# Optimization experiments

Measured on AMD Instinct MI355X. Metric: run time of the kernel, lower is better.

## Reference

```python
import jax, jax.numpy as jnp
import numpy as np

IMG_W, IMG_H = 960.0, 512.0          # NETWORK.IMAGE_SIZE
HM_W, HM_H = 240.0, 128.0            # NETWORK.HEATMAP_SIZE (w, h)
GRID_SIZE = (8000.0, 8000.0, 2000.0)
CUBE = (80, 80, 20)
SPACE_CENTER = (0.0, -500.0, 800.0)


def _make_grid():
    # compute_grid: meshgrid(indexing='ij'), flattened to [nbins, 3]
    gx = np.linspace(-GRID_SIZE[0] / 2, GRID_SIZE[0] / 2, CUBE[0]) + SPACE_CENTER[0]
    gy = np.linspace(-GRID_SIZE[1] / 2, GRID_SIZE[1] / 2, CUBE[1]) + SPACE_CENTER[1]
    gz = np.linspace(-GRID_SIZE[2] / 2, GRID_SIZE[2] / 2, CUBE[2]) + SPACE_CENTER[2]
    X, Y, Z = np.meshgrid(gx, gy, gz, indexing='ij')
    return jnp.asarray(np.stack([X.ravel(), Y.ravel(), Z.ravel()], 1), jnp.float32)


def setup_inputs() -> dict:
    key = jax.random.key(0)
    ks = jax.random.split(key, 8)
    n, B, J, H, W = 5, 4, 15, 128, 240
    heatmaps = jax.random.uniform(ks[0], (n, B, J, H, W), jnp.float32)
    # cameras: rotate about z per view, positioned so all grid points have depth > 0
    thetas = np.linspace(0.0, 2 * np.pi, n, endpoint=False)
    Rs = np.zeros((n, B, 3, 3), np.float32)
    for v, th in enumerate(thetas):
        c, s = np.cos(th), np.sin(th)
        Rs[v, :] = np.array([[c, -s, 0.0], [s, c, 0.0], [0.0, 0.0, 1.0]], np.float32)
    cam_R = jnp.asarray(Rs)
    cam_T = jnp.asarray(np.tile(np.array([0.0, 0.0, -5000.0], np.float32), (n, B, 1))) \
        + 50.0 * jax.random.normal(ks[1], (n, B, 3), jnp.float32)
    cam_f = 1500.0 + 20.0 * jax.random.normal(ks[2], (n, B, 2), jnp.float32)
    cam_c = jnp.asarray([IMG_W / 2, IMG_H / 2], jnp.float32) \
        + 5.0 * jax.random.normal(ks[3], (n, B, 2), jnp.float32)
    cam_k = jnp.asarray(np.tile(np.array([-0.01, 0.001, 0.0], np.float32), (n, B, 1))) \
        + 1e-4 * jax.random.normal(ks[4], (n, B, 3), jnp.float32)
    cam_p = 1e-3 * jax.random.normal(ks[5], (n, B, 2), jnp.float32)
    center = jnp.asarray([IMG_W / 2, IMG_H / 2], jnp.float32) \
        + 10.0 * jax.random.normal(ks[6], (n, B, 2), jnp.float32)
    scale = jnp.asarray([IMG_W / 200.0, IMG_H / 200.0], jnp.float32) \
        * (1.0 + 0.05 * jax.random.uniform(ks[7], (n, B, 2), jnp.float32))
    return {"heatmaps": heatmaps, "cam_R": cam_R, "cam_T": cam_T, "cam_f": cam_f,
            "cam_c": cam_c, "cam_k": cam_k, "cam_p": cam_p, "center": center,
            "scale": scale}


def _forward(heatmaps, cam_R, cam_T, cam_f, cam_c, cam_k, cam_p, center, scale):
    n, B, J, Hd, Wd = heatmaps.shape
    grid = _make_grid()                                   # [N, 3]
    N = grid.shape[0]
    # --- project_pose (pinhole + radial/tangential distortion) ---
    diff = grid[None, None] - cam_T[:, :, None, :]        # [v,b,N,3]
    xcam = jnp.einsum('vbij,vbnj->vbni', cam_R, diff)     # [v,b,N,3]
    y = xcam[..., :2] / (xcam[..., 2:3] + 1e-5)
    r2 = jnp.sum(y * y, -1)                               # [v,b,N]
    radial = 1.0 + cam_k[..., 0:1] * r2 + cam_k[..., 1:2] * r2 ** 2 + cam_k[..., 2:3] * r2 ** 3
    tan = cam_p[..., 0:1] * y[..., 1] + cam_p[..., 1:2] * y[..., 0]
    y = y * (radial + 2.0 * tan)[..., None] \
        + jnp.stack([cam_p[..., 1], cam_p[..., 0]], -1)[:, :, None, :] * r2[..., None]
    pix = cam_f[:, :, None, :] * y + cam_c[:, :, None, :]  # [v,b,N,2]
    # --- bounding: inside image of size (width, height) = 2*center ---
    wh = 2.0 * center                                      # [v,b,2]
    bounding = ((pix[..., 0] >= 0) & (pix[..., 1] >= 0)
                & (pix[..., 0] < wh[..., 0:1]) & (pix[..., 1] < wh[..., 1:2])
                ).astype(heatmaps.dtype)                   # [v,b,N]
    maxwh = jnp.maximum(wh[..., 0], wh[..., 1])[..., None, None]
    pix = jnp.clip(pix, -1.0, maxwh)
    # --- get_transform(center, scale, 0, img_size) + do_transform ---
    hs = 200.0 * scale                                     # [v,b,2]
    img = jnp.asarray([IMG_W, IMG_H], heatmaps.dtype)
    t_scale = img / hs                                     # diag of affine
    t_off = img * (-center / hs + 0.5)
    xy = pix * t_scale[:, :, None, :] + t_off[:, :, None, :]
    # scale to heatmap resolution, then to normalized [-1,1] (align_corners=True)
    xy = xy * (jnp.asarray([HM_W, HM_H], heatmaps.dtype) / img)
    sg = xy / jnp.asarray([HM_W - 1, HM_H - 1], heatmaps.dtype) * 2.0 - 1.0
    sg = jnp.clip(sg, -1.1, 1.1)
    # --- bilinear grid_sample, align_corners=True, zeros padding ---
    px = (sg[..., 0] + 1.0) * 0.5 * (Wd - 1)
    py = (sg[..., 1] + 1.0) * 0.5 * (Hd - 1)
    x0 = jnp.floor(px)
    y0 = jnp.floor(py)
    wx = px - x0
    wy = py - y0
    x0i = x0.astype(jnp.int32)
    y0i = y0.astype(jnp.int32)
    flat = heatmaps.reshape(n, B, J, Hd * Wd)

    def corner(xi, yi):
        valid = ((xi >= 0) & (xi < Wd) & (yi >= 0) & (yi < Hd)).astype(heatmaps.dtype)
        idx = jnp.clip(yi, 0, Hd - 1) * Wd + jnp.clip(xi, 0, Wd - 1)   # [v,b,N]
        g = jnp.take_along_axis(flat, idx[:, :, None, :], axis=3)       # [v,b,J,N]
        return g * valid[:, :, None, :]

    val = (corner(x0i, y0i) * ((1 - wx) * (1 - wy))[:, :, None, :]
           + corner(x0i + 1, y0i) * (wx * (1 - wy))[:, :, None, :]
           + corner(x0i, y0i + 1) * ((1 - wx) * wy)[:, :, None, :]
           + corner(x0i + 1, y0i + 1) * (wx * wy)[:, :, None, :])       # [v,b,J,N]
    # --- per-view cube = bounding * sampled; combine over views ---
    cubes_v = bounding[:, :, None, :] * val
    num = jnp.sum(cubes_v * bounding[:, :, None, :], axis=0)            # [b,J,N]
    den = jnp.sum(bounding, axis=0)[:, None, :] + 1e-6
    cubes = jnp.clip(num / den, 0.0, 1.0).reshape(B, J, CUBE[0], CUBE[1], CUBE[2])
    grids = jnp.broadcast_to(grid, (B, N, 3))
    return cubes, grids


def reference(heatmaps, cam_R, cam_T, cam_f, cam_c, cam_k, cam_p, center, scale):
    return _forward(heatmaps, cam_R, cam_T, cam_f, cam_c, cam_k, cam_p, center, scale)
```

## Files before the change

### kernel.cpp

```cpp
#include <hip/hip_runtime.h>
#include <hip/hip_fp16.h>

#define NV 5
#define NB 4
#define NJ 15
#define HD 128
#define WD 240
#define CX 80
#define CY 80
#define CZ 20
#define NPTS (CX*CY*CZ)
#define JP16 16
#define BLOCKS_PER_B (NPTS/256)
#define NWG (NB*BLOCKS_PER_B)

struct ViewSample {
    float w[4];
    int   cx0, cx1, cy0, cy1;
    float bnd;
};

__device__ __forceinline__ ViewSample project_one_view(
    float gx, float gy, float gz,
    const float* __restrict__ cam_R, const float* __restrict__ cam_T,
    const float* __restrict__ cam_f, const float* __restrict__ cam_c,
    const float* __restrict__ cam_k, const float* __restrict__ cam_p,
    const float* __restrict__ center, const float* __restrict__ scale,
    int cb)
{
    const float* R = cam_R + cb*9;
    const float* T = cam_T + cb*3;
    float fx = cam_f[cb*2+0], fy = cam_f[cb*2+1];
    float ccx = cam_c[cb*2+0], ccy = cam_c[cb*2+1];
    float k0 = cam_k[cb*3+0], k1 = cam_k[cb*3+1], k2 = cam_k[cb*3+2];
    float p0 = cam_p[cb*2+0], p1 = cam_p[cb*2+1];
    float cenx = center[cb*2+0], ceny = center[cb*2+1];
    float scx = scale[cb*2+0],  scy = scale[cb*2+1];

    float dx = gx - T[0], dy = gy - T[1], dz = gz - T[2];
    float xc = R[0]*dx + R[1]*dy + R[2]*dz;
    float yc = R[3]*dx + R[4]*dy + R[5]*dz;
    float zc = R[6]*dx + R[7]*dy + R[8]*dz;
    float invz = 1.0f / (zc + 1e-5f);
    float ux = xc * invz, uy = yc * invz;
    float r2 = ux*ux + uy*uy;
    float radial = 1.0f + k0*r2 + k1*(r2*r2) + k2*(r2*r2*r2);
    float tn = p0*uy + p1*ux;
    float m  = radial + 2.0f*tn;
    float xd = ux*m + p1*r2;
    float yd = uy*m + p0*r2;
    float pixx = fx*xd + ccx;
    float pixy = fy*yd + ccy;

    float whx = 2.0f*cenx, why = 2.0f*ceny;
    float bnd = (pixx >= 0.0f && pixy >= 0.0f && pixx < whx && pixy < why) ? 1.0f : 0.0f;
    float mwh = fmaxf(whx, why);
    pixx = fminf(fmaxf(pixx, -1.0f), mwh);
    pixy = fminf(fmaxf(pixy, -1.0f), mwh);

    float hsx = 200.0f*scx, hsy = 200.0f*scy;
    float xyx = (pixx * (960.0f/hsx) + 960.0f*(-cenx/hsx + 0.5f)) * 0.25f;
    float xyy = (pixy * (512.0f/hsy) + 512.0f*(-ceny/hsy + 0.5f)) * 0.25f;
    float sgx = (xyx / 239.0f) * 2.0f - 1.0f;
    float sgy = (xyy / 127.0f) * 2.0f - 1.0f;
    sgx = fminf(fmaxf(sgx, -1.1f), 1.1f);
    sgy = fminf(fmaxf(sgy, -1.1f), 1.1f);

    float pxf = (sgx + 1.0f) * 0.5f * 239.0f;
    float pyf = (sgy + 1.0f) * 0.5f * 127.0f;
    float x0f = floorf(pxf), y0f = floorf(pyf);
    float wx = pxf - x0f, wy = pyf - y0f;
    int x0 = (int)x0f, y0 = (int)y0f;
    int x1 = x0 + 1,   y1 = y0 + 1;
    float vx0 = (x0 >= 0 && x0 < WD) ? 1.0f : 0.0f;
    float vx1 = (x1 >= 0 && x1 < WD) ? 1.0f : 0.0f;
    float vy0 = (y0 >= 0 && y0 < HD) ? 1.0f : 0.0f;
    float vy1 = (y1 >= 0 && y1 < HD) ? 1.0f : 0.0f;

    ViewSample s;
    s.cx0 = min(max(x0, 0), WD-1);
    s.cx1 = min(max(x1, 0), WD-1);
    s.cy0 = min(max(y0, 0), HD-1);
    s.cy1 = min(max(y1, 0), HD-1);
    s.w[0] = (1.0f-wx)*(1.0f-wy) * vx0*vy0 * bnd;
    s.w[1] = wx*(1.0f-wy)        * vx1*vy0 * bnd;
    s.w[2] = (1.0f-wx)*wy        * vx0*vy1 * bnd;
    s.w[3] = wx*wy               * vx1*vy1 * bnd;
    s.bnd = bnd;
    return s;
}

__device__ __forceinline__ void grid_coords(int nn, float& gx, float& gy, float& gz) {
    int iz = nn % CZ;
    int iy = (nn / CZ) % CY;
    int ix = nn / (CZ*CY);
    gx = (float)(((double)ix * (8000.0/79.0) - 4000.0) + 0.0);
    gy = (float)(((double)iy * (8000.0/79.0) - 4000.0) - 500.0);
    gz = (float)(((double)iz * (2000.0/19.0) - 1000.0) + 800.0);
}

__global__ __launch_bounds__(256) void hm_transpose_f16(
    const float* __restrict__ hm, __half* __restrict__ out)
{
    int idx = blockIdx.x * 256 + threadIdx.x;
    if (idx >= NV*NB*HD*WD) return;
    int x  = idx % WD;
    int y  = (idx / WD) % HD;
    int vb = idx / (WD*HD);
    const float* src = hm + ((size_t)vb*NJ*HD + (size_t)y)*WD + x;
    union { float4 f4[2]; __half h[16]; } u;
    #pragma unroll
    for (int j = 0; j < NJ; ++j) u.h[j] = __float2half(src[(size_t)j*HD*WD]);
    u.h[15] = __float2half(0.0f);
    float4* dst = reinterpret_cast<float4*>(out + (size_t)idx * JP16);
    dst[0] = u.f4[0];
    dst[1] = u.f4[1];
}

__global__ __launch_bounds__(256) void project_kernel_f16(
    const __half* __restrict__ hmT,
    const float* __restrict__ cam_R, const float* __restrict__ cam_T,
    const float* __restrict__ cam_f, const float* __restrict__ cam_c,
    const float* __restrict__ cam_k, const float* __restrict__ cam_p,
    const float* __restrict__ center, const float* __restrict__ scale,
    float* __restrict__ out_cubes, float* __restrict__ out_grids)
{
    int wg   = (int)blockIdx.x;
    int swz  = (wg % 8) * (NWG/8) + wg / 8;
    const int b  = swz / BLOCKS_PER_B;
    const int nn = (swz % BLOCKS_PER_B)*256 + threadIdx.x;

    float gx, gy, gz;
    grid_coords(nn, gx, gy, gz);

    float wts[NV][4];
    int   offs[NV][4];
    float den = 0.0f;

    #pragma unroll
    for (int v = 0; v < NV; ++v) {
        int cb = v*NB + b;
        ViewSample s = project_one_view(gx, gy, gz, cam_R, cam_T, cam_f, cam_c,
                                        cam_k, cam_p, center, scale, cb);
        wts[v][0] = s.w[0]; wts[v][1] = s.w[1];
        wts[v][2] = s.w[2]; wts[v][3] = s.w[3];
        int base = cb * (HD*WD*JP16);
        offs[v][0] = base + (s.cy0*WD + s.cx0)*JP16;
        offs[v][1] = base + (s.cy0*WD + s.cx1)*JP16;
        offs[v][2] = base + (s.cy1*WD + s.cx0)*JP16;
        offs[v][3] = base + (s.cy1*WD + s.cx1)*JP16;
        den += s.bnd;
    }

    float acc[NJ];
    #pragma unroll
    for (int j = 0; j < NJ; ++j) acc[j] = 0.0f;

    #pragma unroll
    for (int v = 0; v < NV; ++v) {
        #pragma unroll
        for (int c = 0; c < 4; ++c) {
            float w = wts[v][c];
            union { float4 f4[2]; __half2 h2[8]; } u;
            const float4* p = reinterpret_cast<const float4*>(hmT + offs[v][c]);
            u.f4[0] = p[0];
            u.f4[1] = p[1];
            #pragma unroll
            for (int k = 0; k < 7; ++k) {
                float2 f = __half22float2(u.h2[k]);
                acc[2*k]   += w * f.x;
                acc[2*k+1] += w * f.y;
            }
            float2 f7 = __half22float2(u.h2[7]);
            acc[14] += w * f7.x;
        }
    }

    float inv_den = 1.0f / (den + 1e-6f);
    #pragma unroll
    for (int j = 0; j < NJ; ++j) {
        float val = fminf(fmaxf(acc[j]*inv_den, 0.0f), 1.0f);
        out_cubes[((size_t)b*NJ + j)*NPTS + nn] = val;
    }
    float* g = out_grids + ((size_t)b*NPTS + nn)*3;
    g[0] = gx; g[1] = gy; g[2] = gz;
}

__global__ __launch_bounds__(256) void project_kernel_direct(
    const float* __restrict__ hm,
    const float* __restrict__ cam_R, const float* __restrict__ cam_T,
    const float* __restrict__ cam_f, const float* __restrict__ cam_c,
    const float* __restrict__ cam_k, const float* __restrict__ cam_p,
    const float* __restrict__ center, const float* __restrict__ scale,
    float* __restrict__ out_cubes, float* __restrict__ out_grids)
{
    const int b  = blockIdx.x / BLOCKS_PER_B;
    const int nn = (blockIdx.x % BLOCKS_PER_B)*256 + threadIdx.x;

    float gx, gy, gz;
    grid_coords(nn, gx, gy, gz);

    float wts[NV][4];
    int   offs[NV][4];
    float den = 0.0f;

    #pragma unroll
    for (int v = 0; v < NV; ++v) {
        int cb = v*NB + b;
        ViewSample s = project_one_view(gx, gy, gz, cam_R, cam_T, cam_f, cam_c,
                                        cam_k, cam_p, center, scale, cb);
        wts[v][0] = s.w[0]; wts[v][1] = s.w[1];
        wts[v][2] = s.w[2]; wts[v][3] = s.w[3];
        offs[v][0] = s.cy0*WD + s.cx0;
        offs[v][1] = s.cy0*WD + s.cx1;
        offs[v][2] = s.cy1*WD + s.cx0;
        offs[v][3] = s.cy1*WD + s.cx1;
        den += s.bnd;
    }

    float acc[NJ];
    #pragma unroll
    for (int j = 0; j < NJ; ++j) acc[j] = 0.0f;

    #pragma unroll
    for (int v = 0; v < NV; ++v) {
        int cb = v*NB + b;
        #pragma unroll
        for (int j = 0; j < NJ; ++j) {
            const float* base = hm + ((size_t)cb*NJ + j)*(HD*WD);
            acc[j] += wts[v][0]*base[offs[v][0]] + wts[v][1]*base[offs[v][1]]
                    + wts[v][2]*base[offs[v][2]] + wts[v][3]*base[offs[v][3]];
        }
    }

    float inv_den = 1.0f / (den + 1e-6f);
    #pragma unroll
    for (int j = 0; j < NJ; ++j) {
        float val = fminf(fmaxf(acc[j]*inv_den, 0.0f), 1.0f);
        out_cubes[((size_t)b*NJ + j)*NPTS + nn] = val;
    }
    float* g = out_grids + ((size_t)b*NPTS + nn)*3;
    g[0] = gx; g[1] = gy; g[2] = gz;
}

extern "C" void kernel_launch(void* const* d_in, const int* in_sizes, int n_in,
                              void* d_out, int out_size, void* d_ws, size_t ws_size,
                              hipStream_t stream) {
    const float* hm     = (const float*)d_in[0];
    const float* cam_R  = (const float*)d_in[1];
    const float* cam_T  = (const float*)d_in[2];
    const float* cam_f  = (const float*)d_in[3];
    const float* cam_c  = (const float*)d_in[4];
    const float* cam_k  = (const float*)d_in[5];
    const float* cam_p  = (const float*)d_in[6];
    const float* center = (const float*)d_in[7];
    const float* scale  = (const float*)d_in[8];

    float* out_cubes = (float*)d_out;
    float* out_grids = out_cubes + (size_t)NB*NJ*NPTS;

    size_t need = (size_t)NV*NB*HD*WD*JP16*sizeof(__half);
    if (ws_size >= need) {
        __half* hmT = (__half*)d_ws;
        hipLaunchKernelGGL(hm_transpose_f16,
                           dim3((NV*NB*HD*WD)/256), dim3(256), 0, stream, hm, hmT);
        hipLaunchKernelGGL(project_kernel_f16,
                           dim3(NWG), dim3(256), 0, stream,
                           hmT, cam_R, cam_T, cam_f, cam_c, cam_k, cam_p,
                           center, scale, out_cubes, out_grids);
    } else {
        hipLaunchKernelGGL(project_kernel_direct,
                           dim3(NWG), dim3(256), 0, stream,
                           hm, cam_R, cam_T, cam_f, cam_c, cam_k, cam_p,
                           center, scale, out_cubes, out_grids);
    }
}
```

Before: 126.7 us.

## Drop fp16 transpose pass and gather directly from fp32 heatmaps with skip

Removes the separate transpose-to-fp16 kernel and its workspace, gathering bilinear corners straight from the original fp32 [v,b,J,H,W] heatmaps inside a single fused kernel. The view loop is no longer unrolled, and a wave-level __any test skips the gathers for views where no lane in the wave has nonzero weight. This avoids the extra launch and the full read and write of the transposed buffer, but each point now issues 60 scattered scalar loads per view instead of two vectorized 16-byte loads per corner. Keeping fp32 also avoids the fp16 rounding of the heatmap values.

```diff
diff --git a/kernel.cpp b/kernel.cpp
--- a/kernel.cpp
+++ b/kernel.cpp
@@ -1,5 +1,4 @@
 #include <hip/hip_runtime.h>
-#include <hip/hip_fp16.h>
 
 #define NV 5
 #define NB 4
@@ -10,7 +9,6 @@
 #define CY 80
 #define CZ 20
 #define NPTS (CX*CY*CZ)
-#define JP16 16
 #define BLOCKS_PER_B (NPTS/256)
 #define NWG (NB*BLOCKS_PER_B)
 
@@ -99,26 +97,8 @@
     gz = (float)(((double)iz * (2000.0/19.0) - 1000.0) + 800.0);
 }
 
-__global__ __launch_bounds__(256) void hm_transpose_f16(
-    const float* __restrict__ hm, __half* __restrict__ out)
-{
-    int idx = blockIdx.x * 256 + threadIdx.x;
-    if (idx >= NV*NB*HD*WD) return;
-    int x  = idx % WD;
-    int y  = (idx / WD) % HD;
-    int vb = idx / (WD*HD);
-    const float* src = hm + ((size_t)vb*NJ*HD + (size_t)y)*WD + x;
-    union { float4 f4[2]; __half h[16]; } u;
-    #pragma unroll
-    for (int j = 0; j < NJ; ++j) u.h[j] = __float2half(src[(size_t)j*HD*WD]);
-    u.h[15] = __float2half(0.0f);
-    float4* dst = reinterpret_cast<float4*>(out + (size_t)idx * JP16);
-    dst[0] = u.f4[0];
-    dst[1] = u.f4[1];
-}
-
-__global__ __launch_bounds__(256) void project_kernel_f16(
-    const __half* __restrict__ hmT,
+__global__ __launch_bounds__(256) void project_kernel_fused(
+    const float* __restrict__ hm,
     const float* __restrict__ cam_R, const float* __restrict__ cam_T,
     const float* __restrict__ cam_f, const float* __restrict__ cam_c,
     const float* __restrict__ cam_k, const float* __restrict__ cam_p,
@@ -133,103 +113,32 @@
     float gx, gy, gz;
     grid_coords(nn, gx, gy, gz);
 
-    float wts[NV][4];
-    int   offs[NV][4];
+    float acc[NJ];
+    #pragma unroll
+    for (int j = 0; j < NJ; ++j) acc[j] = 0.0f;
     float den = 0.0f;
 
-    #pragma unroll
+    #pragma unroll 1
     for (int v = 0; v < NV; ++v) {
         int cb = v*NB + b;
         ViewSample s = project_one_view(gx, gy, gz, cam_R, cam_T, cam_f, cam_c,
                                         cam_k, cam_p, center, scale, cb);
-        wts[v][0] = s.w[0]; wts[v][1] = s.w[1];
-        wts[v][2] = s.w[2]; wts[v][3] = s.w[3];
-        int base = cb * (HD*WD*JP16);
-        offs[v][0] = base + (s.cy0*WD + s.cx0)*JP16;
-        offs[v][1] = base + (s.cy0*WD + s.cx1)*JP16;
-        offs[v][2] = base + (s.cy1*WD + s.cx0)*JP16;
-        offs[v][3] = base + (s.cy1*WD + s.cx1)*JP16;
         den += s.bnd;
-    }
-
-    float acc[NJ];
-    #pragma unroll
-    for (int j = 0; j < NJ; ++j) acc[j] = 0.0f;
-
-    #pragma unroll
-    for (int v = 0; v < NV; ++v) {
-        #pragma unroll
-        for (int c = 0; c < 4; ++c) {
-            float w = wts[v][c];
-            union { float4 f4[2]; __half2 h2[8]; } u;
-            const float4* p = reinterpret_cast<const float4*>(hmT + offs[v][c]);
-            u.f4[0] = p[0];
-            u.f4[1] = p[1];
-            #pragma unroll
-            for (int k = 0; k < 7; ++k) {
-                float2 f = __half22float2(u.h2[k]);
-                acc[2*k]   += w * f.x;
-                acc[2*k+1] += w * f.y;
+        float wsum = s.w[0] + s.w[1] + s.w[2] + s.w[3];
+        if (__any(wsum > 0.0f)) {
+            if (wsum > 0.0f) {
+                int o00 = s.cy0*WD + s.cx0;
+                int o10 = s.cy0*WD + s.cx1;
+                int o01 = s.cy1*WD + s.cx0;
+                int o11 = s.cy1*WD + s.cx1;
+                const float* base = hm + (size_t)cb*NJ*(HD*WD);
+                #pragma unroll
+                for (int j = 0; j < NJ; ++j) {
+                    const float* p = base + (size_t)j*(HD*WD);
+                    acc[j] += s.w[0]*p[o00] + s.w[1]*p[o10]
+                            + s.w[2]*p[o01] + s.w[3]*p[o11];
+                }
             }
-            float2 f7 = __half22float2(u.h2[7]);
-            acc[14] += w * f7.x;
-        }
-    }
-
-    float inv_den = 1.0f / (den + 1e-6f);
-    #pragma unroll
-    for (int j = 0; j < NJ; ++j) {
-        float val = fminf(fmaxf(acc[j]*inv_den, 0.0f), 1.0f);
-        out_cubes[((size_t)b*NJ + j)*NPTS + nn] = val;
-    }
-    float* g = out_grids + ((size_t)b*NPTS + nn)*3;
-    g[0] = gx; g[1] = gy; g[2] = gz;
-}
-
-__global__ __launch_bounds__(256) void project_kernel_direct(
-    const float* __restrict__ hm,
-    const float* __restrict__ cam_R, const float* __restrict__ cam_T,
-    const float* __restrict__ cam_f, const float* __restrict__ cam_c,
-    const float* __restrict__ cam_k, const float* __restrict__ cam_p,
-    const float* __restrict__ center, const float* __restrict__ scale,
-    float* __restrict__ out_cubes, float* __restrict__ out_grids)
-{
-    const int b  = blockIdx.x / BLOCKS_PER_B;
-    const int nn = (blockIdx.x % BLOCKS_PER_B)*256 + threadIdx.x;
-
-    float gx, gy, gz;
-    grid_coords(nn, gx, gy, gz);
-
-    float wts[NV][4];
-    int   offs[NV][4];
-    float den = 0.0f;
-
-    #pragma unroll
-    for (int v = 0; v < NV; ++v) {
-        int cb = v*NB + b;
-        ViewSample s = project_one_view(gx, gy, gz, cam_R, cam_T, cam_f, cam_c,
-                                        cam_k, cam_p, center, scale, cb);
-        wts[v][0] = s.w[0]; wts[v][1] = s.w[1];
-        wts[v][2] = s.w[2]; wts[v][3] = s.w[3];
-        offs[v][0] = s.cy0*WD + s.cx0;
-        offs[v][1] = s.cy0*WD + s.cx1;
-        offs[v][2] = s.cy1*WD + s.cx0;
-        offs[v][3] = s.cy1*WD + s.cx1;
-        den += s.bnd;
-    }
-
-    float acc[NJ];
-    #pragma unroll
-    for (int j = 0; j < NJ; ++j) acc[j] = 0.0f;
-
-    #pragma unroll
-    for (int v = 0; v < NV; ++v) {
-        int cb = v*NB + b;
-        #pragma unroll
-        for (int j = 0; j < NJ; ++j) {
-            const float* base = hm + ((size_t)cb*NJ + j)*(HD*WD);
-            acc[j] += wts[v][0]*base[offs[v][0]] + wts[v][1]*base[offs[v][1]]
-                    + wts[v][2]*base[offs[v][2]] + wts[v][3]*base[offs[v][3]];
         }
     }
 
@@ -259,19 +168,8 @@
     float* out_cubes = (float*)d_out;
     float* out_grids = out_cubes + (size_t)NB*NJ*NPTS;
 
-    size_t need = (size_t)NV*NB*HD*WD*JP16*sizeof(__half);
-    if (ws_size >= need) {
-        __half* hmT = (__half*)d_ws;
-        hipLaunchKernelGGL(hm_transpose_f16,
-                           dim3((NV*NB*HD*WD)/256), dim3(256), 0, stream, hm, hmT);
-        hipLaunchKernelGGL(project_kernel_f16,
-                           dim3(NWG), dim3(256), 0, stream,
-                           hmT, cam_R, cam_T, cam_f, cam_c, cam_k, cam_p,
-                           center, scale, out_cubes, out_grids);
-    } else {
-        hipLaunchKernelGGL(project_kernel_direct,
-                           dim3(NWG), dim3(256), 0, stream,
-                           hm, cam_R, cam_T, cam_f, cam_c, cam_k, cam_p,
-                           center, scale, out_cubes, out_grids);
-    }
+    hipLaunchKernelGGL(project_kernel_fused,
+                       dim3(NWG), dim3(256), 0, stream,
+                       hm, cam_R, cam_T, cam_f, cam_c, cam_k, cam_p,
+                       center, scale, out_cubes, out_grids);
 }
```

After: 147.6 us. +16.4%, slower.
